# Performance work log

Hardware: AMD Instinct MI355X
Metric: run time of the kernel (lower is better)

The kernel has to match this reference:

```python
import jax, jax.numpy as jnp
import numpy as np

B, S, D = 4, 2048, 1024
H, HD = 16, 64
FF = 4096
EPS = 1e-5
NEG = -1000000.0


def setup_inputs() -> dict:
    key = jax.random.key(0)
    ks = jax.random.split(key, 12)
    sc = lambda n: 1.0 / np.sqrt(n)
    return {
        "x": jax.random.normal(ks[0], (B, S, D), jnp.float32),
        "valid_lens": jax.random.randint(ks[1], (B,), 1, S, jnp.int32),
        "Wq": jax.random.normal(ks[2], (D, H * HD), jnp.float32) * sc(D),
        "Wk": jax.random.normal(ks[3], (D, H * HD), jnp.float32) * sc(D),
        "Wv": jax.random.normal(ks[4], (D, H * HD), jnp.float32) * sc(D),
        "Wo": jax.random.normal(ks[5], (H * HD, D), jnp.float32) * sc(H * HD),
        "W1": jax.random.normal(ks[6], (D, FF), jnp.float32) * sc(D),
        "b1": jnp.zeros((FF,), jnp.float32),
        "W2": jax.random.normal(ks[7], (FF, D), jnp.float32) * sc(FF),
        "b2": jnp.zeros((D,), jnp.float32),
        "g1": jnp.ones((D,), jnp.float32),
        "beta1": jnp.zeros((D,), jnp.float32),
        "g2": jnp.ones((D,), jnp.float32),
        "beta2": jnp.zeros((D,), jnp.float32),
    }


def _layernorm(x, g, b):
    mu = jnp.mean(x, axis=-1, keepdims=True)
    var = jnp.var(x, axis=-1, keepdims=True)
    return (x - mu) * jax.lax.rsqrt(var + EPS) * g + b


def _encoder_block(x, valid_lens, Wq, Wk, Wv, Wo, W1, b1, W2, b2, g1, beta1, g2, beta2):
    # multi-head attention (vectorized over heads; masked softmax as in original)
    q = (x @ Wq).reshape(B, S, H, HD)
    k = (x @ Wk).reshape(B, S, H, HD)
    v = (x @ Wv).reshape(B, S, H, HD)
    scores = jnp.einsum("bqhd,bkhd->bhqk", q, k) / np.sqrt(HD)
    # mask: key positions >= valid_len[b] set to -1e6 (matches python-loop masking)
    col = jnp.arange(S)[None, None, None, :]           # [1,1,1,S]
    mask = col < valid_lens[:, None, None, None]       # [B,1,1,S]
    scores = jnp.where(mask, scores, NEG)
    w = jax.nn.softmax(scores, axis=-1)
    attn = jnp.einsum("bhqk,bkhd->bqhd", w, v).reshape(B, S, H * HD)
    attn_out = attn @ Wo
    res1 = _layernorm(attn_out + x, g1, beta1)
    ff = jax.nn.relu(res1 @ W1 + b1) @ W2 + b2
    return _layernorm(ff + res1, g2, beta2)


def reference(x, valid_lens, Wq, Wk, Wv, Wo, W1, b1, W2, b2, g1, beta1, g2, beta2):
    return _encoder_block(x, valid_lens, Wq, Wk, Wv, Wo, W1, b1, W2, b2, g1, beta1, g2, beta2)
```

## Files before the change

kernel.cpp:

```cpp
#include <hip/hip_runtime.h>
#include <hip/hip_bf16.h>
#include <stdint.h>

#define BB 4
#define SS 2048
#define DD 1024
#define HH 16
#define HD 64
#define FF 4096
#define MM (BB * SS)
#define BH (BB * HH)

typedef __bf16 bf16x8 __attribute__((ext_vector_type(8)));
typedef float f32x4 __attribute__((ext_vector_type(4)));

static __device__ __forceinline__ unsigned short f2bf(float f) {
  union { float f; unsigned u; } v; v.f = f;
  unsigned r = v.u + 0x7fffu + ((v.u >> 16) & 1u);
  return (unsigned short)(r >> 16);
}

static __device__ __forceinline__ unsigned packbf2(float a, float b) {
  __hip_bfloat162 h = __float22bfloat162_rn(float2{a, b});
  union { __hip_bfloat162 h; unsigned u; } cv; cv.h = h; return cv.u;
}

#define GLD_LDS16(SRC, DST)                                          \
  __builtin_amdgcn_global_load_lds(                                  \
      (const __attribute__((address_space(1))) void*)(SRC),          \
      (__attribute__((address_space(3))) void*)(DST), 16, 0, 0)

__global__ __launch_bounds__(256) void cast_bf16_k(const float* __restrict__ in,
                                                   unsigned short* __restrict__ out) {
  size_t i = ((size_t)blockIdx.x * 256 + threadIdx.x) * 4;
  float4 v = *(const float4*)(in + i);
  ushort4 u;
  u.x = f2bf(v.x); u.y = f2bf(v.y); u.z = f2bf(v.z); u.w = f2bf(v.w);
  *(ushort4*)(out + i) = u;
}

__global__ __launch_bounds__(256) void transpose_cast_k(const float* __restrict__ in,
                                                        unsigned short* __restrict__ out,
                                                        int K, int N) {
  __shared__ float tile[32][33];
  int n0 = blockIdx.x * 32, k0 = blockIdx.y * 32;
  int tx = threadIdx.x, ty = threadIdx.y;
#pragma unroll
  for (int i = 0; i < 32; i += 8)
    tile[ty + i][tx] = in[(size_t)(k0 + ty + i) * N + n0 + tx];
  __syncthreads();
#pragma unroll
  for (int i = 0; i < 32; i += 8)
    out[(size_t)(n0 + ty + i) * K + k0 + tx] = f2bf(tile[tx][ty + i]);
}

template <int EPI>
__global__ __launch_bounds__(256, 2) void gemm_bt(const unsigned short* __restrict__ A,
                                                  const unsigned short* __restrict__ BT,
                                                  const float* __restrict__ bias,
                                                  void* __restrict__ Cout,
                                                  int N, int K) {
  __shared__ __align__(16) unsigned short Al[128 * 64];
  __shared__ __align__(16) unsigned short Bl[128 * 64];
  const int t = threadIdx.x;
  const int w = t >> 6, l = t & 63, lr = l & 15, lg = l >> 4;
  const int gx = gridDim.x;
  int lin = blockIdx.y * gx + blockIdx.x;
  const int nb = gx * gridDim.y;
  lin = (lin & 7) * (nb >> 3) + (lin >> 3);
  const int brow = (lin / gx) << 7, bcol = (lin % gx) << 7;
  const int wr = w >> 1, wc = w & 1;
  f32x4 acc[4][4] = {};

  for (int kt = 0; kt < K; kt += 64) {
    __syncthreads();
#pragma unroll
    for (int is = 0; is < 4; ++is) {
      int c = is * 256 + t;
      int row = c >> 3;
      int js = (c & 7) ^ (row & 7);
      GLD_LDS16(A + (size_t)(brow + row) * K + kt + js * 8,
                &Al[(size_t)(is * 256 + w * 64) * 8]);
      GLD_LDS16(BT + (size_t)(bcol + row) * K + kt + js * 8,
                &Bl[(size_t)(is * 256 + w * 64) * 8]);
    }
    __syncthreads();
#pragma unroll
    for (int kk = 0; kk < 2; ++kk) {
      bf16x8 af[4], bfr[4];
#pragma unroll
      for (int m = 0; m < 4; ++m) {
        int row = wr * 64 + m * 16 + lr;
        af[m] = *(const bf16x8*)&Al[row * 64 + (((kk * 4 + lg) ^ (row & 7)) << 3)];
      }
#pragma unroll
      for (int n = 0; n < 4; ++n) {
        int row = wc * 64 + n * 16 + lr;
        bfr[n] = *(const bf16x8*)&Bl[row * 64 + (((kk * 4 + lg) ^ (row & 7)) << 3)];
      }
#pragma unroll
      for (int m = 0; m < 4; ++m)
#pragma unroll
        for (int n = 0; n < 4; ++n)
          acc[m][n] = __builtin_amdgcn_mfma_f32_16x16x32_bf16(af[m], bfr[n], acc[m][n], 0, 0, 0);
    }
  }

#pragma unroll
  for (int m = 0; m < 4; ++m) {
#pragma unroll
    for (int n = 0; n < 4; ++n) {
      int col = bcol + wc * 64 + n * 16 + lr;
      float bv = 0.f;
      if (EPI == 3 || EPI == 4) bv = bias[col];
#pragma unroll
      for (int i = 0; i < 4; ++i) {
        int row = brow + wr * 64 + m * 16 + lg * 4 + i;
        float v = acc[m][n][i];
        if (EPI == 0) {
          ((float*)Cout)[(size_t)row * N + col] = v;
        } else if (EPI == 3) {
          v += bv; v = v > 0.f ? v : 0.f;
          ((unsigned short*)Cout)[(size_t)row * N + col] = f2bf(v);
        } else if (EPI == 4) {
          v += bv;
          ((float*)Cout)[(size_t)row * N + col] = v;
        } else if (EPI == 5) {
          int b = row >> 11, s = row & 2047;
          int which = col >> 10, cin = col & 1023;
          int h = cin >> 6, hd = cin & 63;
          unsigned short* qb = (unsigned short*)Cout;
          if (which == 0) {
            qb[(((size_t)(b * HH + h)) * SS + s) * HD + hd] = f2bf(v * 0.125f);
          } else if (which == 1) {
            (qb + (size_t)MM * DD)[(((size_t)(b * HH + h)) * SS + s) * HD + hd] = f2bf(v);
          } else {
            (qb + 2 * (size_t)MM * DD)[(((size_t)(b * HH + h)) * HD + hd) * SS + s] = f2bf(v);
          }
        }
      }
    }
  }
}

__global__ __launch_bounds__(256, 4) void attn_kernel(const unsigned short* __restrict__ Q,
                                                      const unsigned short* __restrict__ Kg,
                                                      const unsigned short* __restrict__ VT,
                                                      const int* __restrict__ vlens,
                                                      unsigned short* __restrict__ O) {
  __shared__ __align__(16) unsigned short Kt[64 * 64];
  __shared__ __align__(16) unsigned short Vt[64 * 64];
  const int t = threadIdx.x;
  const int w = t >> 6, l = t & 63, lr = l & 15, lg = l >> 4;
  const int gid = blockIdx.x;
  const int bh = gid & 63, qb = gid >> 6;
  const int b = bh >> 4, h = bh & 15;
  const int q0 = qb << 6;
  const int vl = vlens[b];
  const size_t base = (size_t)bh * SS * HD;

  bf16x8 qf[2];
  {
    const int qrow = q0 + w * 16 + lr;
    qf[0] = *(const bf16x8*)(Q + base + (size_t)qrow * HD + lg * 8);
    qf[1] = *(const bf16x8*)(Q + base + (size_t)qrow * HD + 32 + lg * 8);
  }
  f32x4 o[4] = {};
  float m_r = -3.0e38f, l_r = 0.f;

  const int nkv = (vl + 63) >> 6;
  for (int kbi = 0; kbi < nkv; ++kbi) {
    const int kb = kbi << 6;
    __syncthreads();
#pragma unroll
    for (int is = 0; is < 2; ++is) {
      int c = is * 256 + t;
      int row = c >> 3;
      int js = (c & 7) ^ (row & 7);
      GLD_LDS16(Kg + base + (size_t)(kb + row) * HD + js * 8,
                &Kt[(is * 256 + w * 64) * 8]);
      GLD_LDS16(VT + base + (size_t)row * SS + kb + js * 8,
                &Vt[(is * 256 + w * 64) * 8]);
    }
    __syncthreads();

    f32x4 s[4] = {};
    __builtin_amdgcn_s_setprio(1);
#pragma unroll
    for (int kk = 0; kk < 2; ++kk)
#pragma unroll
      for (int n = 0; n < 4; ++n) {
        int row = n * 16 + lr;
        bf16x8 kf = *(const bf16x8*)&Kt[row * 64 + (((kk * 4 + lg) ^ (row & 7)) << 3)];
        s[n] = __builtin_amdgcn_mfma_f32_16x16x32_bf16(kf, qf[kk], s[n], 0, 0, 0);
      }
    __builtin_amdgcn_s_setprio(0);

    float sv[16];
    const int kbase = kb + lg * 4;
#pragma unroll
    for (int n = 0; n < 4; ++n)
#pragma unroll
      for (int i = 0; i < 4; ++i) {
        float v = s[n][i];
        if (kbase + n * 16 + i >= vl) v = -1.0e30f;
        sv[n * 4 + i] = v;
      }
    float tm[16];
#pragma unroll
    for (int j = 0; j < 16; ++j) tm[j] = sv[j];
#pragma unroll
    for (int st = 8; st >= 1; st >>= 1)
#pragma unroll
      for (int j = 0; j < 8; ++j)
        if (j < st) tm[j] = fmaxf(tm[j], tm[j + st]);
    float rm = tm[0];
    rm = fmaxf(rm, __shfl_xor(rm, 16));
    rm = fmaxf(rm, __shfl_xor(rm, 32));

    if (__any(rm > m_r + 8.f)) {
      float mnew = fmaxf(m_r, rm);
      float alpha = __expf(m_r - mnew);
      m_r = mnew;
      l_r *= alpha;
      float af[4];
#pragma unroll
      for (int i = 0; i < 4; ++i) af[i] = __shfl(alpha, lg * 4 + i);
#pragma unroll
      for (int n = 0; n < 4; ++n)
#pragma unroll
        for (int i = 0; i < 4; ++i) o[n][i] *= af[i];
    }

    float p[16];
#pragma unroll
    for (int j = 0; j < 16; ++j) p[j] = __expf(sv[j] - m_r);
    float ts[16];
#pragma unroll
    for (int j = 0; j < 16; ++j) ts[j] = p[j];
#pragma unroll
    for (int st = 8; st >= 1; st >>= 1)
#pragma unroll
      for (int j = 0; j < 8; ++j)
        if (j < st) ts[j] += ts[j + st];
    float rs = ts[0];
    rs += __shfl_xor(rs, 16);
    rs += __shfl_xor(rs, 32);
    l_r += rs;

    unsigned pd[4][2];
#pragma unroll
    for (int n = 0; n < 4; ++n) {
      pd[n][0] = packbf2(p[n * 4 + 0], p[n * 4 + 1]);
      pd[n][1] = packbf2(p[n * 4 + 2], p[n * 4 + 3]);
    }

#pragma unroll
    for (int kk = 0; kk < 2; ++kk) {
      unsigned pa[4];
#pragma unroll
      for (int jj = 0; jj < 4; ++jj) {
        int src = lr + 16 * (2 * (lg & 1) + (jj >> 1));
        unsigned rlo = __shfl(pd[2 * kk + 0][jj & 1], src);
        unsigned rhi = __shfl(pd[2 * kk + 1][jj & 1], src);
        pa[jj] = (lg & 2) ? rhi : rlo;
      }
      union { unsigned u[4]; bf16x8 v; } pb;
      pb.u[0] = pa[0]; pb.u[1] = pa[1]; pb.u[2] = pa[2]; pb.u[3] = pa[3];
      __builtin_amdgcn_s_setprio(1);
#pragma unroll
      for (int nd = 0; nd < 4; ++nd) {
        int row = nd * 16 + lr;
        bf16x8 vf = *(const bf16x8*)&Vt[row * 64 + (((kk * 4 + lg) ^ (row & 7)) << 3)];
        o[nd] = __builtin_amdgcn_mfma_f32_16x16x32_bf16(pb.v, vf, o[nd], 0, 0, 0);
      }
      __builtin_amdgcn_s_setprio(0);
    }
  }

  float linv[4];
#pragma unroll
  for (int i = 0; i < 4; ++i) linv[i] = 1.f / __shfl(l_r, lg * 4 + i);
#pragma unroll
  for (int nd = 0; nd < 4; ++nd)
#pragma unroll
    for (int i = 0; i < 4; ++i) {
      int qrow = q0 + w * 16 + lg * 4 + i;
      O[((size_t)b * SS + qrow) * DD + h * HD + nd * 16 + lr] = f2bf(o[nd][i] * linv[i]);
    }
}

__global__ __launch_bounds__(256) void ln_kernel(const float* __restrict__ a,
                                                 const float* __restrict__ bsrc,
                                                 const float* __restrict__ g,
                                                 const float* __restrict__ be,
                                                 float* __restrict__ outf,
                                                 unsigned short* __restrict__ outb) {
  const int row = blockIdx.x;
  const int t = threadIdx.x;
  const float4 av = ((const float4*)(a + (size_t)row * DD))[t];
  const float4 bv = ((const float4*)(bsrc + (size_t)row * DD))[t];
  float4 s;
  s.x = av.x + bv.x; s.y = av.y + bv.y; s.z = av.z + bv.z; s.w = av.w + bv.w;
  float sum = s.x + s.y + s.z + s.w;
  float sq = s.x * s.x + s.y * s.y + s.z * s.z + s.w * s.w;
#pragma unroll
  for (int mm = 1; mm < 64; mm <<= 1) {
    sum += __shfl_xor(sum, mm);
    sq += __shfl_xor(sq, mm);
  }
  __shared__ float red[8];
  const int w = t >> 6, l = t & 63;
  if (l == 0) { red[w] = sum; red[4 + w] = sq; }
  __syncthreads();
  sum = red[0] + red[1] + red[2] + red[3];
  sq = red[4] + red[5] + red[6] + red[7];
  const float mu = sum * (1.f / (float)DD);
  const float var = sq * (1.f / (float)DD) - mu * mu;
  const float rs = rsqrtf(var + 1e-5f);
  const float4 gv = ((const float4*)g)[t];
  const float4 bev = ((const float4*)be)[t];
  float4 y;
  y.x = (s.x - mu) * rs * gv.x + bev.x;
  y.y = (s.y - mu) * rs * gv.y + bev.y;
  y.z = (s.z - mu) * rs * gv.z + bev.z;
  y.w = (s.w - mu) * rs * gv.w + bev.w;
  if (outf) ((float4*)(outf + (size_t)row * DD))[t] = y;
  if (outb) {
    ushort4 u;
    u.x = f2bf(y.x); u.y = f2bf(y.y); u.z = f2bf(y.z); u.w = f2bf(y.w);
    ((ushort4*)(outb + (size_t)row * DD))[t] = u;
  }
}

extern "C" void kernel_launch(void* const* d_in, const int* in_sizes, int n_in,
                              void* d_out, int out_size, void* d_ws, size_t ws_size,
                              hipStream_t stream) {
  (void)in_sizes; (void)n_in; (void)out_size; (void)ws_size;
  const float* x = (const float*)d_in[0];
  const int* vlen = (const int*)d_in[1];
  const float* Wq = (const float*)d_in[2];
  const float* Wk = (const float*)d_in[3];
  const float* Wv = (const float*)d_in[4];
  const float* Wo = (const float*)d_in[5];
  const float* W1 = (const float*)d_in[6];
  const float* b1 = (const float*)d_in[7];
  const float* W2 = (const float*)d_in[8];
  const float* b2 = (const float*)d_in[9];
  const float* g1 = (const float*)d_in[10];
  const float* be1 = (const float*)d_in[11];
  const float* g2 = (const float*)d_in[12];
  const float* be2 = (const float*)d_in[13];
  float* out = (float*)d_out;

  char* ws = (char*)d_ws;
  size_t off = 0;
  auto alloc = [&](size_t bytes) {
    char* p = ws + off;
    off += (bytes + 255) & ~(size_t)255;
    return p;
  };
  unsigned short* xb = (unsigned short*)alloc((size_t)MM * DD * 2);
  unsigned short* WqT = (unsigned short*)alloc((size_t)DD * DD * 2);
  unsigned short* WkT = (unsigned short*)alloc((size_t)DD * DD * 2);
  unsigned short* WvT = (unsigned short*)alloc((size_t)DD * DD * 2);
  unsigned short* WoT = (unsigned short*)alloc((size_t)DD * DD * 2);
  unsigned short* W1T = (unsigned short*)alloc((size_t)FF * DD * 2);
  unsigned short* W2T = (unsigned short*)alloc((size_t)DD * FF * 2);
  unsigned short* Qb = (unsigned short*)alloc((size_t)MM * DD * 2);
  unsigned short* Kbb = (unsigned short*)alloc((size_t)MM * DD * 2);
  unsigned short* VTb = (unsigned short*)alloc((size_t)MM * DD * 2);
  unsigned short* attnb = (unsigned short*)alloc((size_t)MM * DD * 2);
  float* proj = (float*)alloc((size_t)MM * DD * 4);
  float* res1f = (float*)alloc((size_t)MM * DD * 4);
  unsigned short* res1b = (unsigned short*)alloc((size_t)MM * DD * 2);
  unsigned short* ff1 = Qb;
  float* ff2 = proj;
  (void)Kbb; (void)VTb;

  cast_bf16_k<<<MM * DD / 1024, 256, 0, stream>>>(x, xb);
  transpose_cast_k<<<dim3(32, 32), dim3(32, 8), 0, stream>>>(Wq, WqT, DD, DD);
  transpose_cast_k<<<dim3(32, 32), dim3(32, 8), 0, stream>>>(Wk, WkT, DD, DD);
  transpose_cast_k<<<dim3(32, 32), dim3(32, 8), 0, stream>>>(Wv, WvT, DD, DD);
  transpose_cast_k<<<dim3(32, 32), dim3(32, 8), 0, stream>>>(Wo, WoT, DD, DD);
  transpose_cast_k<<<dim3(128, 32), dim3(32, 8), 0, stream>>>(W1, W1T, DD, FF);
  transpose_cast_k<<<dim3(32, 128), dim3(32, 8), 0, stream>>>(W2, W2T, FF, DD);

  gemm_bt<5><<<dim3(24, 64), 256, 0, stream>>>(xb, WqT, nullptr, Qb, 3072, DD);

  attn_kernel<<<dim3(2048), 256, 0, stream>>>(Qb, Kbb, VTb, vlen, attnb);

  gemm_bt<0><<<dim3(8, 64), 256, 0, stream>>>(attnb, WoT, nullptr, proj, DD, DD);
  ln_kernel<<<MM, 256, 0, stream>>>(proj, x, g1, be1, res1f, res1b);
  gemm_bt<3><<<dim3(32, 64), 256, 0, stream>>>(res1b, W1T, b1, ff1, FF, DD);
  gemm_bt<4><<<dim3(8, 64), 256, 0, stream>>>(ff1, W2T, b2, ff2, DD, FF);
  ln_kernel<<<MM, 256, 0, stream>>>(ff2, res1f, g2, be2, out, nullptr);
}
```

Baseline: 450.2 us.

## Use 256-row double-buffered GEMM tiles with 8 waves and MFMA priority

Replaces the 128x128 single-buffered GEMM with a 256xBN tile kernel using 512 threads (8 waves) and double-buffered LDS. The next K-slice loads while the current one is computed, and s_setprio raises priority around the MFMA block. Larger tiles raise operand reuse and cut global traffic per FLOP. In exchange, LDS use (up to 128KB for BN=256) and accumulator registers grow, which risks lower occupancy or spills. The smaller grids may also underfill the CUs on the N=1024 GEMMs.

```diff
diff --git a/kernel.cpp b/kernel.cpp
--- a/kernel.cpp
+++ b/kernel.cpp
@@ -54,68 +54,86 @@
     out[(size_t)(n0 + ty + i) * K + k0 + tx] = f2bf(tile[tx][ty + i]);
 }
 
-template <int EPI>
-__global__ __launch_bounds__(256, 2) void gemm_bt(const unsigned short* __restrict__ A,
+template <int EPI, int BN>
+__global__ __launch_bounds__(512, 2) void gemm256(const unsigned short* __restrict__ A,
                                                   const unsigned short* __restrict__ BT,
                                                   const float* __restrict__ bias,
                                                   void* __restrict__ Cout,
                                                   int N, int K) {
-  __shared__ __align__(16) unsigned short Al[128 * 64];
-  __shared__ __align__(16) unsigned short Bl[128 * 64];
+  constexpr int BM = 256;
+  constexpr int WN = BN / 4;
+  constexpr int NR = WN / 16;
+  constexpr int BCH = BN * 64 / 8 / 512;
+  __shared__ __align__(16) unsigned short Al[2][BM * 64];
+  __shared__ __align__(16) unsigned short Bl[2][BN * 64];
   const int t = threadIdx.x;
   const int w = t >> 6, l = t & 63, lr = l & 15, lg = l >> 4;
+  const int wr = w >> 2, wc = w & 3;
   const int gx = gridDim.x;
   int lin = blockIdx.y * gx + blockIdx.x;
   const int nb = gx * gridDim.y;
   lin = (lin & 7) * (nb >> 3) + (lin >> 3);
-  const int brow = (lin / gx) << 7, bcol = (lin % gx) << 7;
-  const int wr = w >> 1, wc = w & 1;
-  f32x4 acc[4][4] = {};
-
-  for (int kt = 0; kt < K; kt += 64) {
-    __syncthreads();
-#pragma unroll
-    for (int is = 0; is < 4; ++is) {
-      int c = is * 256 + t;
+  const int brow = (lin / gx) * BM, bcol = (lin % gx) * BN;
+  f32x4 acc[8][NR] = {};
+
+  auto stage = [&](int buf, int kt) {
+#pragma unroll
+    for (int i = 0; i < 4; ++i) {
+      int c = i * 512 + t;
       int row = c >> 3;
       int js = (c & 7) ^ (row & 7);
-      GLD_LDS16(A + (size_t)(brow + row) * K + kt + js * 8,
-                &Al[(size_t)(is * 256 + w * 64) * 8]);
-      GLD_LDS16(BT + (size_t)(bcol + row) * K + kt + js * 8,
-                &Bl[(size_t)(is * 256 + w * 64) * 8]);
-    }
+      GLD_LDS16(A + (size_t)(brow + row) * K + kt * 64 + js * 8,
+                &Al[buf][(i * 512 + w * 64) * 8]);
+    }
+#pragma unroll
+    for (int i = 0; i < BCH; ++i) {
+      int c = i * 512 + t;
+      int row = c >> 3;
+      int js = (c & 7) ^ (row & 7);
+      GLD_LDS16(BT + (size_t)(bcol + row) * K + kt * 64 + js * 8,
+                &Bl[buf][(i * 512 + w * 64) * 8]);
+    }
+  };
+
+  const int nk = K >> 6;
+  stage(0, 0);
+  for (int kt = 0; kt < nk; ++kt) {
+    const int cur = kt & 1;
     __syncthreads();
+    if (kt + 1 < nk) stage(cur ^ 1, kt + 1);
 #pragma unroll
     for (int kk = 0; kk < 2; ++kk) {
-      bf16x8 af[4], bfr[4];
-#pragma unroll
-      for (int m = 0; m < 4; ++m) {
-        int row = wr * 64 + m * 16 + lr;
-        af[m] = *(const bf16x8*)&Al[row * 64 + (((kk * 4 + lg) ^ (row & 7)) << 3)];
-      }
-#pragma unroll
-      for (int n = 0; n < 4; ++n) {
-        int row = wc * 64 + n * 16 + lr;
-        bfr[n] = *(const bf16x8*)&Bl[row * 64 + (((kk * 4 + lg) ^ (row & 7)) << 3)];
-      }
-#pragma unroll
-      for (int m = 0; m < 4; ++m)
-#pragma unroll
-        for (int n = 0; n < 4; ++n)
+      bf16x8 af[8], bfr[NR];
+#pragma unroll
+      for (int m = 0; m < 8; ++m) {
+        int row = wr * 128 + m * 16 + lr;
+        af[m] = *(const bf16x8*)&Al[cur][row * 64 + (((kk * 4 + lg) ^ (row & 7)) << 3)];
+      }
+#pragma unroll
+      for (int n = 0; n < NR; ++n) {
+        int row = wc * WN + n * 16 + lr;
+        bfr[n] = *(const bf16x8*)&Bl[cur][row * 64 + (((kk * 4 + lg) ^ (row & 7)) << 3)];
+      }
+      __builtin_amdgcn_s_setprio(1);
+#pragma unroll
+      for (int m = 0; m < 8; ++m)
+#pragma unroll
+        for (int n = 0; n < NR; ++n)
           acc[m][n] = __builtin_amdgcn_mfma_f32_16x16x32_bf16(af[m], bfr[n], acc[m][n], 0, 0, 0);
-    }
-  }
-
-#pragma unroll
-  for (int m = 0; m < 4; ++m) {
-#pragma unroll
-    for (int n = 0; n < 4; ++n) {
-      int col = bcol + wc * 64 + n * 16 + lr;
+      __builtin_amdgcn_s_setprio(0);
+    }
+  }
+
+#pragma unroll
+  for (int m = 0; m < 8; ++m) {
+#pragma unroll
+    for (int n = 0; n < NR; ++n) {
+      int col = bcol + wc * WN + n * 16 + lr;
       float bv = 0.f;
       if (EPI == 3 || EPI == 4) bv = bias[col];
 #pragma unroll
       for (int i = 0; i < 4; ++i) {
-        int row = brow + wr * 64 + m * 16 + lg * 4 + i;
+        int row = brow + wr * 128 + m * 16 + lg * 4 + i;
         float v = acc[m][n][i];
         if (EPI == 0) {
           ((float*)Cout)[(size_t)row * N + col] = v;
@@ -386,13 +404,13 @@
   transpose_cast_k<<<dim3(128, 32), dim3(32, 8), 0, stream>>>(W1, W1T, DD, FF);
   transpose_cast_k<<<dim3(32, 128), dim3(32, 8), 0, stream>>>(W2, W2T, FF, DD);
 
-  gemm_bt<5><<<dim3(24, 64), 256, 0, stream>>>(xb, WqT, nullptr, Qb, 3072, DD);
+  gemm256<5, 128><<<dim3(24, 32), 512, 0, stream>>>(xb, WqT, nullptr, Qb, 3072, DD);
 
   attn_kernel<<<dim3(2048), 256, 0, stream>>>(Qb, Kbb, VTb, vlen, attnb);
 
-  gemm_bt<0><<<dim3(8, 64), 256, 0, stream>>>(attnb, WoT, nullptr, proj, DD, DD);
+  gemm256<0, 128><<<dim3(8, 32), 512, 0, stream>>>(attnb, WoT, nullptr, proj, DD, DD);
   ln_kernel<<<MM, 256, 0, stream>>>(proj, x, g1, be1, res1f, res1b);
-  gemm_bt<3><<<dim3(32, 64), 256, 0, stream>>>(res1b, W1T, b1, ff1, FF, DD);
-  gemm_bt<4><<<dim3(8, 64), 256, 0, stream>>>(ff1, W2T, b2, ff2, DD, FF);
+  gemm256<3, 256><<<dim3(16, 32), 512, 0, stream>>>(res1b, W1T, b1, ff1, FF, DD);
+  gemm256<4, 128><<<dim3(8, 32), 512, 0, stream>>>(ff1, W2T, b2, ff2, DD, FF);
   ln_kernel<<<MM, 256, 0, stream>>>(ff2, res1f, g2, be2, out, nullptr);
 }
```

After: 465.3 us. 1.03x slower.
